# Kernel tuning notes

Measured on AMD Instinct MI355X. Metric: run time of the kernel, lower is better.

Reference implementation:

```python
import jax, jax.numpy as jnp
import numpy as np

B, N2, N3, N4 = 128, 1024, 256, 64
D, H, MLP = 128, 2, 512
EPS = 1e-5


def _sinusoid(n, d):
    pos = np.arange(n, dtype=np.float64)[:, None]
    i = np.arange(d)[None, :]
    ang = pos / np.power(10000.0, 2.0 * (i // 2) / d)
    tab = np.where(i % 2 == 0, np.sin(ang), np.cos(ang))
    return jnp.asarray(tab[None], jnp.float32)  # [1, n, d]


def setup_inputs() -> dict:
    key = jax.random.key(0)
    ks = jax.random.split(key, 16)
    s = 0.02
    inp = {
        "f2": jax.random.normal(ks[0], (B, N2, D), jnp.float32),
        "f3": jax.random.normal(ks[1], (B, N3, D), jnp.float32),
        "f4": jax.random.normal(ks[2], (B, N4, D), jnp.float32),
        "pe2": _sinusoid(N2, D),
        "pe3": _sinusoid(N3, D),
        "pe4": _sinusoid(N4, D),
        "ln1_w": jnp.ones((D,), jnp.float32), "ln1_b": jnp.zeros((D,), jnp.float32),
        "ln2_w": jnp.ones((D,), jnp.float32), "ln2_b": jnp.zeros((D,), jnp.float32),
        "ln3_w": jnp.ones((D,), jnp.float32), "ln3_b": jnp.zeros((D,), jnp.float32),
        "ln4_w": jnp.ones((D,), jnp.float32), "ln4_b": jnp.zeros((D,), jnp.float32),
        "q1_w": s * jax.random.normal(ks[3], (D, D), jnp.float32), "q1_b": jnp.zeros((D,), jnp.float32),
        "k1_w": s * jax.random.normal(ks[4], (D, D), jnp.float32), "k1_b": jnp.zeros((D,), jnp.float32),
        "v1_w": s * jax.random.normal(ks[5], (D, D), jnp.float32), "v1_b": jnp.zeros((D,), jnp.float32),
        "q2_w": s * jax.random.normal(ks[6], (D, D), jnp.float32), "q2_b": jnp.zeros((D,), jnp.float32),
        "k2_w": s * jax.random.normal(ks[7], (D, D), jnp.float32), "k2_b": jnp.zeros((D,), jnp.float32),
        "v2_w": s * jax.random.normal(ks[8], (D, D), jnp.float32), "v2_b": jnp.zeros((D,), jnp.float32),
        "rp_w": s * jax.random.normal(ks[9], (2 * D, D), jnp.float32), "rp_b": jnp.zeros((D,), jnp.float32),
        "ff1_w": s * jax.random.normal(ks[10], (D, MLP), jnp.float32), "ff1_b": jnp.zeros((MLP,), jnp.float32),
        "ff2_w": s * jax.random.normal(ks[11], (MLP, D), jnp.float32), "ff2_b": jnp.zeros((D,), jnp.float32),
    }
    return inp


def _ln(x, w, b):
    m = x.mean(-1, keepdims=True)
    v = ((x - m) ** 2).mean(-1, keepdims=True)  # biased var, matches torch LayerNorm
    return (x - m) * jax.lax.rsqrt(v + EPS) * w + b


def _eff_attn(q, k, v):
    # q: [B,Nq,D]; k,v: [B,Nk,D]. Linear (efficient) attention:
    # softmax over tokens for Q, softmax over head channels for K.
    b, nq, _ = q.shape
    nk = k.shape[1]
    dh = D // H
    qs = jax.nn.softmax(q.reshape(b, nq, H, dh), axis=1)   # dim=2 in [B,C,N] layout == token axis
    ks = jax.nn.softmax(k.reshape(b, nk, H, dh), axis=3)   # dim=1 in [B,C,N] layout == channel axis
    vs = v.reshape(b, nk, H, dh)
    ctx = jnp.einsum('bnhd,bnhe->bhde', ks, vs)            # [B,H,dh,dh] context
    out = jnp.einsum('bhde,bnhd->bnhe', ctx, qs)           # [B,Nq,H,dh]
    return out.reshape(b, nq, D)


def reference(f2, f3, f4, pe2, pe3, pe4,
              ln1_w, ln1_b, ln2_w, ln2_b, ln3_w, ln3_b, ln4_w, ln4_b,
              q1_w, q1_b, k1_w, k1_b, v1_w, v1_b,
              q2_w, q2_b, k2_w, k2_b, v2_w, v2_b,
              rp_w, rp_b, ff1_w, ff1_b, ff2_w, ff2_b):
    f2n = _ln(f2, ln1_w, ln1_b)
    f3n = _ln(f3, ln2_w, ln2_b)
    f4n = _ln(f4, ln3_w, ln3_b)
    q1 = (f2n + pe2) @ q1_w + q1_b
    q2 = (f2n + pe2) @ q2_w + q2_b
    k3 = (f3n + pe3) @ k1_w + k1_b
    v3 = f3n @ v1_w + v1_b
    k4 = (f4n + pe4) @ k2_w + k2_b
    v4 = f4n @ v2_w + v2_b
    a32 = _eff_attn(q1, k3, v3)
    a42 = _eff_attn(q2, k4, v4)
    attn = jnp.concatenate([a32, a42], axis=-1) @ rp_w + rp_b
    x = f2 + attn
    h = _ln(x, ln4_w, ln4_b)
    h = jax.nn.gelu(h @ ff1_w + ff1_b, approximate=False) @ ff2_w + ff2_b
    return x + h
```

## Files before the change

kernel.cpp:

```cpp
#include <hip/hip_runtime.h>
#include <hip/hip_bf16.h>
#include <math.h>

#define BB 128
#define NN2 1024
#define NN3 256
#define NN4 64
#define DD 128
#define MLPD 512
#define EPSF 1e-5f

typedef short bf16x8 __attribute__((ext_vector_type(8)));
typedef float f32x4 __attribute__((ext_vector_type(4)));

__device__ inline ushort f2b(float x) {
    __hip_bfloat16 h = __float2bfloat16(x);
    return __builtin_bit_cast(ushort, h);
}
__device__ inline float b2f(ushort u) {
    unsigned int v = ((unsigned int)u) << 16;
    return __builtin_bit_cast(float, v);
}
__device__ inline float gelu_f(float u) {
    float t = 0.7978845608f * u + 0.0356774081f * (u * u * u);
    float e = __expf(2.f * t);
    return u - u * __builtin_amdgcn_rcpf(e + 1.f);
}

#define MFMA(a, b, c) __builtin_amdgcn_mfma_f32_16x16x32_bf16((a), (b), (c), 0, 0, 0)

__device__ inline char* swad(char* base, int row, int bytecol, int strideB) {
    return base + (size_t)row * strideB + ((bytecol) ^ ((row & 7) << 4));
}

template <int STRIDE>
__device__ inline void ln_stage(const float* __restrict__ x, long base,
                                const float* __restrict__ w, const float* __restrict__ b,
                                ushort xn[][STRIDE], int t)
{
    int r = t >> 3, l8 = t & 7;
    const float4* xr4 = reinterpret_cast<const float4*>(x + (base + r) * DD);
    float4 v[4];
#pragma unroll
    for (int j = 0; j < 4; ++j) v[j] = xr4[l8 * 4 + j];
    float s = 0.f;
#pragma unroll
    for (int j = 0; j < 4; ++j) s += v[j].x + v[j].y + v[j].z + v[j].w;
#pragma unroll
    for (int m = 1; m <= 4; m <<= 1) s += __shfl_xor(s, m, 64);
    float mean = s * (1.f / 128.f);
    float s2 = 0.f;
#pragma unroll
    for (int j = 0; j < 4; ++j) {
        v[j].x -= mean; v[j].y -= mean; v[j].z -= mean; v[j].w -= mean;
        s2 += v[j].x * v[j].x + v[j].y * v[j].y + v[j].z * v[j].z + v[j].w * v[j].w;
    }
#pragma unroll
    for (int m = 1; m <= 4; m <<= 1) s2 += __shfl_xor(s2, m, 64);
    float rstd = rsqrtf(s2 * (1.f / 128.f) + EPSF);
    int c0 = l8 * 16;
#pragma unroll
    for (int j = 0; j < 4; ++j) {
        int c = c0 + j * 4;
        float o0 = v[j].x * rstd * w[c] + b[c];
        float o1 = v[j].y * rstd * w[c + 1] + b[c + 1];
        float o2 = v[j].z * rstd * w[c + 2] + b[c + 2];
        float o3 = v[j].w * rstd * w[c + 3] + b[c + 3];
        uint2 uu;
        uu.x = (unsigned int)f2b(o0) | ((unsigned int)f2b(o1) << 16);
        uu.y = (unsigned int)f2b(o2) | ((unsigned int)f2b(o3) << 16);
        *reinterpret_cast<uint2*>(&xn[r][c]) = uu;
    }
}

__global__ __launch_bounds__(256) void prep_tw(
    const float* __restrict__ q1w, const float* __restrict__ q2w,
    const float* __restrict__ k1w, const float* __restrict__ v1w,
    const float* __restrict__ k2w, const float* __restrict__ v2w,
    const float* __restrict__ ff1w, const float* __restrict__ ff2w,
    const float* __restrict__ rpw,
    ushort* __restrict__ Wqt, ushort* __restrict__ Wkv3t, ushort* __restrict__ Wkv4t,
    ushort* __restrict__ W1t, ushort* __restrict__ W2t, ushort* __restrict__ RpT)
{
    __shared__ ushort trans[4][64][88];
    int w = threadIdx.x >> 6, l = threadIdx.x & 63;
    int tile = blockIdx.x * 4 + w;
    const float* src; ushort* dst; int K, N, tk, tn;
    if (tile < 24) {
        int job = tile >> 2, rel = tile & 3;
        K = 128; N = 128; tk = rel >> 1; tn = rel & 1;
        if      (job == 0) { src = q1w; dst = Wqt; }
        else if (job == 1) { src = q2w; dst = Wqt + 16384; }
        else if (job == 2) { src = k1w; dst = Wkv3t; }
        else if (job == 3) { src = v1w; dst = Wkv3t + 16384; }
        else if (job == 4) { src = k2w; dst = Wkv4t; }
        else               { src = v2w; dst = Wkv4t + 16384; }
    } else if (tile < 40) {
        int rel = tile - 24; src = ff1w; dst = W1t; K = 128; N = 512; tk = rel >> 3; tn = rel & 7;
    } else if (tile < 56) {
        int rel = tile - 40; src = ff2w; dst = W2t; K = 512; N = 128; tk = rel >> 1; tn = rel & 1;
    } else {
        int rel = tile - 56; src = rpw; dst = RpT; K = 256; N = 128; tk = rel >> 1; tn = rel & 1;
    }
    int k0 = tk * 64, n0 = tn * 64;
#pragma unroll
    for (int i = 0; i < 16; ++i) {
        int kr = i * 4 + (l >> 4), nc = (l & 15) * 4;
        float4 v = *reinterpret_cast<const float4*>(&src[(size_t)(k0 + kr) * N + n0 + nc]);
        trans[w][nc + 0][kr] = f2b(v.x);
        trans[w][nc + 1][kr] = f2b(v.y);
        trans[w][nc + 2][kr] = f2b(v.z);
        trans[w][nc + 3][kr] = f2b(v.w);
    }
    __syncthreads();
#pragma unroll
    for (int i = 0; i < 8; ++i) {
        int nr = i * 8 + (l >> 3), c0 = (l & 7) * 8;
        int4 vv = *reinterpret_cast<const int4*>(&trans[w][nr][c0]);
        *reinterpret_cast<int4*>(&dst[(size_t)(n0 + nr) * K + k0 + c0]) = vv;
    }
}

__global__ __launch_bounds__(256) void prep_pe2(
    const float* __restrict__ pe2, const float* __restrict__ pe3, const float* __restrict__ pe4,
    const ushort* __restrict__ Wqt, const ushort* __restrict__ Wkv3t, const ushort* __restrict__ Wkv4t,
    const float* __restrict__ q1b, const float* __restrict__ q2b,
    const float* __restrict__ k1b, const float* __restrict__ v1b,
    const float* __restrict__ k2b, const float* __restrict__ v2b,
    float* __restrict__ peq, float* __restrict__ pekv3, float* __restrict__ pekv4)
{
    __shared__ ushort xn[32][136];
    int bid = blockIdx.x, t = threadIdx.x;
    const float* pe; const ushort* Wt; float* outp; const float* bl; const float* bh; int hiDot; long tb;
    if (bid < 32)      { pe = pe2; Wt = Wqt;   outp = peq;   bl = q1b; bh = q2b; hiDot = 1; tb = (long)bid * 32; }
    else if (bid < 40) { pe = pe3; Wt = Wkv3t; outp = pekv3; bl = k1b; bh = v1b; hiDot = 0; tb = (long)(bid - 32) * 32; }
    else               { pe = pe4; Wt = Wkv4t; outp = pekv4; bl = k2b; bh = v2b; hiDot = 0; tb = (long)(bid - 40) * 32; }
    {
        int r = t >> 3, l8 = t & 7;
        const float4* pr = reinterpret_cast<const float4*>(pe + (tb + r) * 128);
#pragma unroll
        for (int j = 0; j < 4; ++j) {
            float4 v = pr[l8 * 4 + j];
            int c = l8 * 16 + j * 4;
            uint2 uu;
            uu.x = (unsigned int)f2b(v.x) | ((unsigned int)f2b(v.y) << 16);
            uu.y = (unsigned int)f2b(v.z) | ((unsigned int)f2b(v.w) << 16);
            *reinterpret_cast<uint2*>(&xn[r][c]) = uu;
        }
    }
    __syncthreads();
    int w = t >> 6, l = t & 63, l15 = l & 15, rg = l >> 4;
    f32x4 acc[2][4];
#pragma unroll
    for (int m = 0; m < 2; ++m)
#pragma unroll
        for (int n = 0; n < 4; ++n) acc[m][n] = (f32x4){0.f, 0.f, 0.f, 0.f};
#pragma unroll
    for (int kc = 0; kc < 4; ++kc) {
        bf16x8 a0 = *reinterpret_cast<const bf16x8*>(&xn[l15][kc * 32 + rg * 8]);
        bf16x8 a1 = *reinterpret_cast<const bf16x8*>(&xn[16 + l15][kc * 32 + rg * 8]);
#pragma unroll
        for (int nt = 0; nt < 4; ++nt) {
            bf16x8 bfr = *reinterpret_cast<const bf16x8*>(
                &Wt[(size_t)(w * 64 + nt * 16 + l15) * 128 + kc * 32 + rg * 8]);
            acc[0][nt] = MFMA(a0, bfr, acc[0][nt]);
            acc[1][nt] = MFMA(a1, bfr, acc[1][nt]);
        }
    }
#pragma unroll
    for (int mt = 0; mt < 2; ++mt)
#pragma unroll
        for (int j = 0; j < 4; ++j) {
            int row = mt * 16 + rg * 4 + j;
#pragma unroll
            for (int nt = 0; nt < 4; ++nt) {
                int col = w * 64 + nt * 16 + l15;
                float bias = (col < 128) ? bl[col] : bh[col - 128];
                float v = bias + ((col < 128 || hiDot) ? acc[mt][nt][j] : 0.f);
                outp[(tb + row) * 256 + col] = v;
            }
        }
}

__global__ __launch_bounds__(256) void kv_mfma(
    const float* __restrict__ x, const float* __restrict__ lnw, const float* __restrict__ lnb,
    const ushort* __restrict__ Wt, const float* __restrict__ pekv,
    ushort* __restrict__ kst, ushort* __restrict__ vst, int ntok, int ntok_shift)
{
    __shared__ ushort xn[32][136];
    __shared__ ushort trans[4][64][40];
    int t = threadIdx.x;
    long base = (long)blockIdx.x * 32;
    ln_stage<136>(x, base, lnw, lnb, xn, t);
    __syncthreads();
    int w = t >> 6, l = t & 63, l15 = l & 15, rg = l >> 4;
    f32x4 acc[2][4];
#pragma unroll
    for (int m = 0; m < 2; ++m)
#pragma unroll
        for (int n = 0; n < 4; ++n) acc[m][n] = (f32x4){0.f, 0.f, 0.f, 0.f};
#pragma unroll
    for (int kc = 0; kc < 4; ++kc) {
        bf16x8 a0 = *reinterpret_cast<const bf16x8*>(&xn[l15][kc * 32 + rg * 8]);
        bf16x8 a1 = *reinterpret_cast<const bf16x8*>(&xn[16 + l15][kc * 32 + rg * 8]);
#pragma unroll
        for (int nt = 0; nt < 4; ++nt) {
            bf16x8 bfr = *reinterpret_cast<const bf16x8*>(
                &Wt[(size_t)(w * 64 + nt * 16 + l15) * 128 + kc * 32 + rg * 8]);
            acc[0][nt] = MFMA(a0, bfr, acc[0][nt]);
            acc[1][nt] = MFMA(a1, bfr, acc[1][nt]);
        }
    }
    float val[2][4][4];
#pragma unroll
    for (int mt = 0; mt < 2; ++mt)
#pragma unroll
        for (int j = 0; j < 4; ++j) {
            int row = mt * 16 + rg * 4 + j;
            int tok = (int)((base + row) & (ntok - 1));
#pragma unroll
            for (int nt = 0; nt < 4; ++nt) {
                int col = w * 64 + nt * 16 + l15;
                val[mt][nt][j] = acc[mt][nt][j] + pekv[tok * 256 + col];
            }
        }
    if (w < 2) {
#pragma unroll
        for (int mt = 0; mt < 2; ++mt)
#pragma unroll
            for (int j = 0; j < 4; ++j) {
                float mx = val[mt][0][j];
#pragma unroll
                for (int nt = 1; nt < 4; ++nt) mx = fmaxf(mx, val[mt][nt][j]);
#pragma unroll
                for (int m = 1; m <= 8; m <<= 1) mx = fmaxf(mx, __shfl_xor(mx, m, 64));
                float e[4], se = 0.f;
#pragma unroll
                for (int nt = 0; nt < 4; ++nt) { e[nt] = __expf(val[mt][nt][j] - mx); se += e[nt]; }
#pragma unroll
                for (int m = 1; m <= 8; m <<= 1) se += __shfl_xor(se, m, 64);
                float inv = 1.f / se;
#pragma unroll
                for (int nt = 0; nt < 4; ++nt) val[mt][nt][j] = e[nt] * inv;
            }
    }
#pragma unroll
    for (int mt = 0; mt < 2; ++mt)
#pragma unroll
        for (int nt = 0; nt < 4; ++nt)
#pragma unroll
            for (int j = 0; j < 4; ++j)
                trans[w][nt * 16 + l15][mt * 16 + rg * 4 + j] = f2b(val[mt][nt][j]);
    __syncthreads();
    ushort* dst = (w < 2) ? kst : vst;
    int h = w & 1;
    int b = (int)(base >> ntok_shift);
    int tok0 = (int)(base & (ntok - 1));
    long o = (((long)(b * 2 + h) * 64 + l) * ntok + tok0);
    const int4* src = reinterpret_cast<const int4*>(&trans[w][l][0]);
    int4* dp = reinterpret_cast<int4*>(&dst[o]);
#pragma unroll
    for (int i = 0; i < 4; ++i) dp[i] = src[i];
}

__global__ __launch_bounds__(64) void ctx_mfma(
    const ushort* __restrict__ kst3, const ushort* __restrict__ vst3,
    const ushort* __restrict__ kst4, const ushort* __restrict__ vst4,
    ushort* __restrict__ ctxn)
{
    int bid = blockIdx.x;
    int b = bid >> 2, g = bid & 3;
    const ushort* ks; const ushort* vs; int ntok;
    if (g < 2) { ntok = 256; ks = kst3 + (long)(b * 2 + g) * 64 * 256; vs = vst3 + (long)(b * 2 + g) * 64 * 256; }
    else       { ntok = 64;  ks = kst4 + (long)(b * 2 + (g - 2)) * 64 * 64; vs = vst4 + (long)(b * 2 + (g - 2)) * 64 * 64; }
    int l = threadIdx.x, l15 = l & 15, rg = l >> 4;
    f32x4 acc[4][4];
#pragma unroll
    for (int m = 0; m < 4; ++m)
#pragma unroll
        for (int n = 0; n < 4; ++n) acc[m][n] = (f32x4){0.f, 0.f, 0.f, 0.f};
    for (int kc = 0; kc < (ntok >> 5); ++kc) {
        bf16x8 a[4];
#pragma unroll
        for (int mt = 0; mt < 4; ++mt)
            a[mt] = *reinterpret_cast<const bf16x8*>(&ks[(size_t)(mt * 16 + l15) * ntok + kc * 32 + rg * 8]);
#pragma unroll
        for (int nt = 0; nt < 4; ++nt) {
            bf16x8 bfr = *reinterpret_cast<const bf16x8*>(&vs[(size_t)(nt * 16 + l15) * ntok + kc * 32 + rg * 8]);
#pragma unroll
            for (int mt = 0; mt < 4; ++mt) acc[mt][nt] = MFMA(a[mt], bfr, acc[mt][nt]);
        }
    }
#pragma unroll
    for (int mt = 0; mt < 4; ++mt)
#pragma unroll
        for (int nt = 0; nt < 4; ++nt)
#pragma unroll
            for (int j = 0; j < 4; ++j)
                ctxn[((long)bid * 64 + mt * 16 + rg * 4 + j) * 64 + nt * 16 + l15] = f2b(acc[mt][nt][j]);
}

__global__ __launch_bounds__(512) void q_mfma(
    const float* __restrict__ f2, const float* __restrict__ lnw, const float* __restrict__ lnb,
    const ushort* __restrict__ Wqt, const float* __restrict__ peq,
    ushort* __restrict__ qexp, float* __restrict__ partial)
{
    __shared__ ushort xn[64][136];
    __shared__ ushort qt[64][264];
    int t = threadIdx.x;
    long base = (long)blockIdx.x * 64;
    ln_stage<136>(f2, base, lnw, lnb, xn, t);
    __syncthreads();
    int w = t >> 6, l = t & 63, l15 = l & 15, rg = l >> 4;
    f32x4 acc[4][2];
#pragma unroll
    for (int m = 0; m < 4; ++m)
#pragma unroll
        for (int n = 0; n < 2; ++n) acc[m][n] = (f32x4){0.f, 0.f, 0.f, 0.f};
#pragma unroll
    for (int kc = 0; kc < 4; ++kc) {
        bf16x8 a[4];
#pragma unroll
        for (int m = 0; m < 4; ++m)
            a[m] = *reinterpret_cast<const bf16x8*>(&xn[m * 16 + l15][kc * 32 + rg * 8]);
#pragma unroll
        for (int nt = 0; nt < 2; ++nt) {
            bf16x8 bfr = *reinterpret_cast<const bf16x8*>(
                &Wqt[(size_t)(w * 32 + nt * 16 + l15) * 128 + kc * 32 + rg * 8]);
#pragma unroll
            for (int m = 0; m < 4; ++m) acc[m][nt] = MFMA(a[m], bfr, acc[m][nt]);
        }
    }
    float esum[2] = {0.f, 0.f};
#pragma unroll
    for (int m = 0; m < 4; ++m)
#pragma unroll
        for (int j = 0; j < 4; ++j) {
            int row = m * 16 + rg * 4 + j;
            int tok = (int)((base + row) & (NN2 - 1));
#pragma unroll
            for (int nt = 0; nt < 2; ++nt) {
                int col = w * 32 + nt * 16 + l15;
                float v = acc[m][nt][j] + peq[tok * 256 + col];
                float e = __expf(v);
                qt[row][col] = f2b(e);
                esum[nt] += e;
            }
        }
#pragma unroll
    for (int nt = 0; nt < 2; ++nt) {
        esum[nt] += __shfl_xor(esum[nt], 16, 64);
        esum[nt] += __shfl_xor(esum[nt], 32, 64);
    }
    if (rg == 0) {
        int bidx = blockIdx.x >> 4, chunk = blockIdx.x & 15;
#pragma unroll
        for (int nt = 0; nt < 2; ++nt)
            partial[(size_t)(bidx * 16 + chunk) * 256 + w * 32 + nt * 16 + l15] = esum[nt];
    }
    __syncthreads();
    {
        int r = t >> 3, c0 = (t & 7) * 32;
        const int4* sp = reinterpret_cast<const int4*>(&qt[r][c0]);
        int4* dst = reinterpret_cast<int4*>(&qexp[(base + r) * 256 + c0]);
#pragma unroll
        for (int i = 0; i < 4; ++i) dst[i] = sp[i];
    }
}

__global__ __launch_bounds__(256) void scale_rp(
    const float* __restrict__ partial, const ushort* __restrict__ ctxn,
    const ushort* __restrict__ RpT, ushort* __restrict__ MbT)
{
    __shared__ float rsv[256];
    int b = blockIdx.x, t = threadIdx.x;
    {
        float s = 0.f;
        for (int ch = 0; ch < 16; ++ch) s += partial[((size_t)b * 16 + ch) * 256 + t];
        rsv[t] = 1.f / s;
    }
    __syncthreads();
    int w = t >> 6, l = t & 63, l15 = l & 15, rg = l >> 4;
    const ushort* cb = ctxn + ((long)(b * 4 + w)) * 4096;
    bf16x8 a[4][2];
#pragma unroll
    for (int m = 0; m < 4; ++m) {
        float sc = rsv[w * 64 + m * 16 + l15];
#pragma unroll
        for (int kc = 0; kc < 2; ++kc) {
            bf16x8 raw = *reinterpret_cast<const bf16x8*>(
                &cb[(size_t)(m * 16 + l15) * 64 + kc * 32 + rg * 8]);
#pragma unroll
            for (int i = 0; i < 8; ++i)
                raw[i] = (short)f2b(b2f((ushort)raw[i]) * sc);
            a[m][kc] = raw;
        }
    }
#pragma unroll
    for (int nt = 0; nt < 8; ++nt) {
        f32x4 acc[4];
#pragma unroll
        for (int m = 0; m < 4; ++m) acc[m] = (f32x4){0.f, 0.f, 0.f, 0.f};
#pragma unroll
        for (int kc = 0; kc < 2; ++kc) {
            bf16x8 bfr = *reinterpret_cast<const bf16x8*>(
                &RpT[(size_t)(nt * 16 + l15) * 256 + w * 64 + kc * 32 + rg * 8]);
#pragma unroll
            for (int m = 0; m < 4; ++m) acc[m] = MFMA(a[m][kc], bfr, acc[m]);
        }
        int n = nt * 16 + l15;
#pragma unroll
        for (int m = 0; m < 4; ++m) {
            unsigned int u0 = (unsigned int)f2b(acc[m][0]) | ((unsigned int)f2b(acc[m][1]) << 16);
            unsigned int u1 = (unsigned int)f2b(acc[m][2]) | ((unsigned int)f2b(acc[m][3]) << 16);
            uint2 uu; uu.x = u0; uu.y = u1;
            *reinterpret_cast<uint2*>(&MbT[((long)b * 128 + n) * 256 + w * 64 + m * 16 + rg * 4]) = uu;
        }
    }
}

__global__ __launch_bounds__(512, 4) void attn_mlp(
    const ushort* __restrict__ qexp, const ushort* __restrict__ MbT,
    const float* __restrict__ rpb, const float* __restrict__ f2,
    const float* __restrict__ lnw, const float* __restrict__ lnb,
    const ushort* __restrict__ W1t, const float* __restrict__ ff1b,
    const ushort* __restrict__ W2t, const float* __restrict__ ff2b,
    float* __restrict__ out)
{
    __shared__ __align__(16) char smem[32768];
    char* XN = smem;
    char* R2 = smem + 16384;
    float* Ps = reinterpret_cast<float*>(R2);
    float* Pq = reinterpret_cast<float*>(R2 + 2048);
    float* MR = reinterpret_cast<float*>(R2 + 4096);
    float* RR = reinterpret_cast<float*>(R2 + 4352);
    int t = threadIdx.x;
    long base = (long)blockIdx.x * 64;
    int b = blockIdx.x >> 4;
    int w = t >> 6, l = t & 63, l15 = l & 15, rg = l >> 4;
    int col = w * 16 + l15;

    f32x4 accC[4];
#pragma unroll
    for (int m = 0; m < 4; ++m) accC[m] = (f32x4){0.f, 0.f, 0.f, 0.f};
    {
        const ushort* mb = MbT + (long)b * 128 * 256;
#pragma unroll
        for (int h = 0; h < 2; ++h) {
            {
                int sr = t >> 3, sc = (t & 7) * 32;
                const char* src = (const char*)qexp + (base + sr) * 512 + h * 256 + sc;
                int4 v0 = *reinterpret_cast<const int4*>(src);
                int4 v1 = *reinterpret_cast<const int4*>(src + 16);
                *reinterpret_cast<int4*>(swad(R2, sr, sc, 256)) = v0;
                *reinterpret_cast<int4*>(swad(R2, sr, sc + 16, 256)) = v1;
            }
            __syncthreads();
#pragma unroll
            for (int kc = 0; kc < 4; ++kc) {
                bf16x8 bfr = *reinterpret_cast<const bf16x8*>(
                    &mb[(size_t)col * 256 + h * 128 + kc * 32 + rg * 8]);
#pragma unroll
                for (int m = 0; m < 4; ++m) {
                    bf16x8 a = *reinterpret_cast<const bf16x8*>(
                        swad(R2, m * 16 + l15, (kc * 32 + rg * 8) * 2, 256));
                    accC[m] = MFMA(a, bfr, accC[m]);
                }
            }
            __syncthreads();
        }
    }

    float xres[4][4];
    {
        float bias = rpb[col];
#pragma unroll
        for (int m = 0; m < 4; ++m)
#pragma unroll
            for (int j = 0; j < 4; ++j) {
                int row = m * 16 + rg * 4 + j;
                long g = (base + row) * 128 + col;
                float xv = f2[g] + accC[m][j] + bias;
                xres[m][j] = xv;
                float s = xv, q = xv * xv;
#pragma unroll
                for (int msk = 1; msk <= 8; msk <<= 1) {
                    s += __shfl_xor(s, msk, 64);
                    q += __shfl_xor(q, msk, 64);
                }
                if (l15 == 0) { Ps[row * 8 + w] = s; Pq[row * 8 + w] = q; }
            }
    }
    __syncthreads();
    if (t < 64) {
        float4 s0 = *reinterpret_cast<float4*>(&Ps[t * 8]);
        float4 s1 = *reinterpret_cast<float4*>(&Ps[t * 8 + 4]);
        float4 q0 = *reinterpret_cast<float4*>(&Pq[t * 8]);
        float4 q1 = *reinterpret_cast<float4*>(&Pq[t * 8 + 4]);
        float s = s0.x + s0.y + s0.z + s0.w + s1.x + s1.y + s1.z + s1.w;
        float q = q0.x + q0.y + q0.z + q0.w + q1.x + q1.y + q1.z + q1.w;
        float mean = s * (1.f / 128.f);
        float var = q * (1.f / 128.f) - mean * mean;
        MR[t] = mean;
        RR[t] = rsqrtf(var + EPSF);
    }
    __syncthreads();
    {
        float lw = lnw[col], lb = lnb[col];
#pragma unroll
        for (int m = 0; m < 4; ++m)
#pragma unroll
            for (int j = 0; j < 4; ++j) {
                int row = m * 16 + rg * 4 + j;
                float o = (xres[m][j] - MR[row]) * RR[row] * lw + lb;
                *reinterpret_cast<ushort*>(swad(XN, row, col * 2, 256)) = f2b(o);
            }
    }
    __syncthreads();

    f32x4 accF[4];
#pragma unroll
    for (int m = 0; m < 4; ++m) accF[m] = (f32x4){0.f, 0.f, 0.f, 0.f};
#pragma unroll
    for (int q = 0; q < 4; ++q) {
        {
            f32x4 acc[4];
#pragma unroll
            for (int m = 0; m < 4; ++m) acc[m] = (f32x4){0.f, 0.f, 0.f, 0.f};
#pragma unroll
            for (int kc = 0; kc < 4; ++kc) {
                bf16x8 bfr = *reinterpret_cast<const bf16x8*>(
                    &W1t[(size_t)(q * 128 + col) * 128 + kc * 32 + rg * 8]);
#pragma unroll
                for (int m = 0; m < 4; ++m) {
                    bf16x8 a = *reinterpret_cast<const bf16x8*>(
                        swad(XN, m * 16 + l15, (kc * 32 + rg * 8) * 2, 256));
                    acc[m] = MFMA(a, bfr, acc[m]);
                }
            }
            float b1 = ff1b[q * 128 + col];
#pragma unroll
            for (int m = 0; m < 4; ++m)
#pragma unroll
                for (int j = 0; j < 4; ++j)
                    *reinterpret_cast<ushort*>(swad(R2, m * 16 + rg * 4 + j, col * 2, 256))
                        = f2b(gelu_f(acc[m][j] + b1));
        }
        __syncthreads();
#pragma unroll
        for (int kc = 0; kc < 4; ++kc) {
            bf16x8 bfr = *reinterpret_cast<const bf16x8*>(
                &W2t[(size_t)col * 512 + q * 128 + kc * 32 + rg * 8]);
#pragma unroll
            for (int m = 0; m < 4; ++m) {
                bf16x8 a = *reinterpret_cast<const bf16x8*>(
                    swad(R2, m * 16 + l15, (kc * 32 + rg * 8) * 2, 256));
                accF[m] = MFMA(a, bfr, accF[m]);
            }
        }
        if (q < 3) __syncthreads();
    }
    {
        float b2 = ff2b[col];
#pragma unroll
        for (int m = 0; m < 4; ++m)
#pragma unroll
            for (int j = 0; j < 4; ++j) {
                int row = m * 16 + rg * 4 + j;
                long g = (base + row) * 128 + col;
                out[g] = xres[m][j] + accF[m][j] + b2;
            }
    }
}

extern "C" void kernel_launch(void* const* d_in, const int* in_sizes, int n_in,
                              void* d_out, int out_size, void* d_ws, size_t ws_size,
                              hipStream_t stream) {
    const float* f2   = (const float*)d_in[0];
    const float* f3   = (const float*)d_in[1];
    const float* f4   = (const float*)d_in[2];
    const float* pe2  = (const float*)d_in[3];
    const float* pe3  = (const float*)d_in[4];
    const float* pe4  = (const float*)d_in[5];
    const float* ln1w = (const float*)d_in[6];
    const float* ln1b = (const float*)d_in[7];
    const float* ln2w = (const float*)d_in[8];
    const float* ln2b = (const float*)d_in[9];
    const float* ln3w = (const float*)d_in[10];
    const float* ln3b = (const float*)d_in[11];
    const float* ln4w = (const float*)d_in[12];
    const float* ln4b = (const float*)d_in[13];
    const float* q1w  = (const float*)d_in[14];
    const float* q1b  = (const float*)d_in[15];
    const float* k1w  = (const float*)d_in[16];
    const float* k1b  = (const float*)d_in[17];
    const float* v1w  = (const float*)d_in[18];
    const float* v1b  = (const float*)d_in[19];
    const float* q2w  = (const float*)d_in[20];
    const float* q2b  = (const float*)d_in[21];
    const float* k2w  = (const float*)d_in[22];
    const float* k2b  = (const float*)d_in[23];
    const float* v2w  = (const float*)d_in[24];
    const float* v2b  = (const float*)d_in[25];
    const float* rpw  = (const float*)d_in[26];
    const float* rpb  = (const float*)d_in[27];
    const float* ff1w = (const float*)d_in[28];
    const float* ff1b = (const float*)d_in[29];
    const float* ff2w = (const float*)d_in[30];
    const float* ff2b = (const float*)d_in[31];

    char* ws = (char*)d_ws;
    size_t off = 0;
    ushort* qexp  = (ushort*)(ws + off); off += (size_t)BB * NN2 * 256 * 2;
    ushort* kst3  = (ushort*)(ws + off); off += (size_t)BB * 2 * 64 * NN3 * 2;
    ushort* vst3  = (ushort*)(ws + off); off += (size_t)BB * 2 * 64 * NN3 * 2;
    ushort* kst4  = (ushort*)(ws + off); off += (size_t)BB * 2 * 64 * NN4 * 2;
    ushort* vst4  = (ushort*)(ws + off); off += (size_t)BB * 2 * 64 * NN4 * 2;
    ushort* ctxn  = (ushort*)(ws + off); off += (size_t)BB * 4 * 64 * 64 * 2;
    ushort* MbT   = (ushort*)(ws + off); off += (size_t)BB * 128 * 256 * 2;
    ushort* Wqt   = (ushort*)(ws + off); off += 256 * 128 * 2;
    ushort* Wkv3t = (ushort*)(ws + off); off += 256 * 128 * 2;
    ushort* Wkv4t = (ushort*)(ws + off); off += 256 * 128 * 2;
    ushort* W1t   = (ushort*)(ws + off); off += 512 * 128 * 2;
    ushort* W2t   = (ushort*)(ws + off); off += 128 * 512 * 2;
    ushort* RpT   = (ushort*)(ws + off); off += 128 * 256 * 2;
    float*  peq   = (float*)(ws + off);  off += (size_t)NN2 * 256 * 4;
    float*  pekv3 = (float*)(ws + off);  off += (size_t)NN3 * 256 * 4;
    float*  pekv4 = (float*)(ws + off);  off += (size_t)NN4 * 256 * 4;
    float*  partial = (float*)(ws + off); off += (size_t)BB * 16 * 256 * 4;

    prep_tw<<<16, 256, 0, stream>>>(q1w, q2w, k1w, v1w, k2w, v2w, ff1w, ff2w, rpw,
                                    Wqt, Wkv3t, Wkv4t, W1t, W2t, RpT);
    prep_pe2<<<42, 256, 0, stream>>>(pe2, pe3, pe4, Wqt, Wkv3t, Wkv4t,
                                     q1b, q2b, k1b, v1b, k2b, v2b, peq, pekv3, pekv4);
    kv_mfma<<<BB * NN3 / 32, 256, 0, stream>>>(f3, ln2w, ln2b, Wkv3t, pekv3, kst3, vst3, NN3, 8);
    kv_mfma<<<BB * NN4 / 32, 256, 0, stream>>>(f4, ln3w, ln3b, Wkv4t, pekv4, kst4, vst4, NN4, 6);
    ctx_mfma<<<BB * 4, 64, 0, stream>>>(kst3, vst3, kst4, vst4, ctxn);
    q_mfma<<<BB * NN2 / 64, 512, 0, stream>>>(f2, ln1w, ln1b, Wqt, peq, qexp, partial);
    scale_rp<<<BB, 256, 0, stream>>>(partial, ctxn, RpT, MbT);
    attn_mlp<<<BB * NN2 / 64, 512, 0, stream>>>(qexp, MbT, rpb, f2,
                                                ln4w, ln4b, W1t, ff1b, W2t, ff2b, (float*)d_out);
}
```

Baseline: 247.3 us.

## Merge prep kernels, fuse K/V projection launches, swizzle q_mfma shared memory

Weight transposition and positional-embedding projection now run in one prep launch. The PE projection is a plain per-thread fp32 dot product, which removes the dependency on the transposed weights, and the two K/V projection launches are merged into one. The q_mfma shared buffers are repacked into a 32KB XOR-swizzled layout with no padding, and launch bounds are set to allow 4 blocks per CU. The swizzle generalises to wider row strides. The intent is fewer launches, fewer LDS bank conflicts and higher occupancy, at the cost of a slower scalar PE projection and an extra barrier.

```diff
diff --git a/kernel.cpp b/kernel.cpp
--- a/kernel.cpp
+++ b/kernel.cpp
@@ -30,7 +30,7 @@
 #define MFMA(a, b, c) __builtin_amdgcn_mfma_f32_16x16x32_bf16((a), (b), (c), 0, 0, 0)
 
 __device__ inline char* swad(char* base, int row, int bytecol, int strideB) {
-    return base + (size_t)row * strideB + ((bytecol) ^ ((row & 7) << 4));
+    return base + (size_t)row * strideB + ((bytecol) ^ ((row << 4) & (strideB - 16)));
 }
 
 template <int STRIDE>
@@ -73,124 +73,151 @@
     }
 }
 
-__global__ __launch_bounds__(256) void prep_tw(
+__device__ inline void ln_stage_s(const float* __restrict__ x, long base,
+                                  const float* __restrict__ w, const float* __restrict__ b,
+                                  char* R, int t)
+{
+    int r = t >> 3, l8 = t & 7;
+    const float4* xr4 = reinterpret_cast<const float4*>(x + (base + r) * DD);
+    float4 v[4];
+#pragma unroll
+    for (int j = 0; j < 4; ++j) v[j] = xr4[l8 * 4 + j];
+    float s = 0.f;
+#pragma unroll
+    for (int j = 0; j < 4; ++j) s += v[j].x + v[j].y + v[j].z + v[j].w;
+#pragma unroll
+    for (int m = 1; m <= 4; m <<= 1) s += __shfl_xor(s, m, 64);
+    float mean = s * (1.f / 128.f);
+    float s2 = 0.f;
+#pragma unroll
+    for (int j = 0; j < 4; ++j) {
+        v[j].x -= mean; v[j].y -= mean; v[j].z -= mean; v[j].w -= mean;
+        s2 += v[j].x * v[j].x + v[j].y * v[j].y + v[j].z * v[j].z + v[j].w * v[j].w;
+    }
+#pragma unroll
+    for (int m = 1; m <= 4; m <<= 1) s2 += __shfl_xor(s2, m, 64);
+    float rstd = rsqrtf(s2 * (1.f / 128.f) + EPSF);
+    int c0 = l8 * 16;
+#pragma unroll
+    for (int j = 0; j < 4; ++j) {
+        int c = c0 + j * 4;
+        float o0 = v[j].x * rstd * w[c] + b[c];
+        float o1 = v[j].y * rstd * w[c + 1] + b[c + 1];
+        float o2 = v[j].z * rstd * w[c + 2] + b[c + 2];
+        float o3 = v[j].w * rstd * w[c + 3] + b[c + 3];
+        uint2 uu;
+        uu.x = (unsigned int)f2b(o0) | ((unsigned int)f2b(o1) << 16);
+        uu.y = (unsigned int)f2b(o2) | ((unsigned int)f2b(o3) << 16);
+        *reinterpret_cast<uint2*>(swad(R, r, c * 2, 256)) = uu;
+    }
+}
+
+__global__ __launch_bounds__(256) void prep_all(
     const float* __restrict__ q1w, const float* __restrict__ q2w,
     const float* __restrict__ k1w, const float* __restrict__ v1w,
     const float* __restrict__ k2w, const float* __restrict__ v2w,
     const float* __restrict__ ff1w, const float* __restrict__ ff2w,
     const float* __restrict__ rpw,
-    ushort* __restrict__ Wqt, ushort* __restrict__ Wkv3t, ushort* __restrict__ Wkv4t,
-    ushort* __restrict__ W1t, ushort* __restrict__ W2t, ushort* __restrict__ RpT)
-{
-    __shared__ ushort trans[4][64][88];
-    int w = threadIdx.x >> 6, l = threadIdx.x & 63;
-    int tile = blockIdx.x * 4 + w;
-    const float* src; ushort* dst; int K, N, tk, tn;
-    if (tile < 24) {
-        int job = tile >> 2, rel = tile & 3;
-        K = 128; N = 128; tk = rel >> 1; tn = rel & 1;
-        if      (job == 0) { src = q1w; dst = Wqt; }
-        else if (job == 1) { src = q2w; dst = Wqt + 16384; }
-        else if (job == 2) { src = k1w; dst = Wkv3t; }
-        else if (job == 3) { src = v1w; dst = Wkv3t + 16384; }
-        else if (job == 4) { src = k2w; dst = Wkv4t; }
-        else               { src = v2w; dst = Wkv4t + 16384; }
-    } else if (tile < 40) {
-        int rel = tile - 24; src = ff1w; dst = W1t; K = 128; N = 512; tk = rel >> 3; tn = rel & 7;
-    } else if (tile < 56) {
-        int rel = tile - 40; src = ff2w; dst = W2t; K = 512; N = 128; tk = rel >> 1; tn = rel & 1;
-    } else {
-        int rel = tile - 56; src = rpw; dst = RpT; K = 256; N = 128; tk = rel >> 1; tn = rel & 1;
-    }
-    int k0 = tk * 64, n0 = tn * 64;
-#pragma unroll
-    for (int i = 0; i < 16; ++i) {
-        int kr = i * 4 + (l >> 4), nc = (l & 15) * 4;
-        float4 v = *reinterpret_cast<const float4*>(&src[(size_t)(k0 + kr) * N + n0 + nc]);
-        trans[w][nc + 0][kr] = f2b(v.x);
-        trans[w][nc + 1][kr] = f2b(v.y);
-        trans[w][nc + 2][kr] = f2b(v.z);
-        trans[w][nc + 3][kr] = f2b(v.w);
-    }
-    __syncthreads();
-#pragma unroll
-    for (int i = 0; i < 8; ++i) {
-        int nr = i * 8 + (l >> 3), c0 = (l & 7) * 8;
-        int4 vv = *reinterpret_cast<const int4*>(&trans[w][nr][c0]);
-        *reinterpret_cast<int4*>(&dst[(size_t)(n0 + nr) * K + k0 + c0]) = vv;
-    }
-}
-
-__global__ __launch_bounds__(256) void prep_pe2(
     const float* __restrict__ pe2, const float* __restrict__ pe3, const float* __restrict__ pe4,
-    const ushort* __restrict__ Wqt, const ushort* __restrict__ Wkv3t, const ushort* __restrict__ Wkv4t,
     const float* __restrict__ q1b, const float* __restrict__ q2b,
     const float* __restrict__ k1b, const float* __restrict__ v1b,
     const float* __restrict__ k2b, const float* __restrict__ v2b,
+    ushort* __restrict__ Wqt, ushort* __restrict__ Wkv3t, ushort* __restrict__ Wkv4t,
+    ushort* __restrict__ W1t, ushort* __restrict__ W2t, ushort* __restrict__ RpT,
     float* __restrict__ peq, float* __restrict__ pekv3, float* __restrict__ pekv4)
 {
-    __shared__ ushort xn[32][136];
-    int bid = blockIdx.x, t = threadIdx.x;
-    const float* pe; const ushort* Wt; float* outp; const float* bl; const float* bh; int hiDot; long tb;
-    if (bid < 32)      { pe = pe2; Wt = Wqt;   outp = peq;   bl = q1b; bh = q2b; hiDot = 1; tb = (long)bid * 32; }
-    else if (bid < 40) { pe = pe3; Wt = Wkv3t; outp = pekv3; bl = k1b; bh = v1b; hiDot = 0; tb = (long)(bid - 32) * 32; }
-    else               { pe = pe4; Wt = Wkv4t; outp = pekv4; bl = k2b; bh = v2b; hiDot = 0; tb = (long)(bid - 40) * 32; }
-    {
-        int r = t >> 3, l8 = t & 7;
-        const float4* pr = reinterpret_cast<const float4*>(pe + (tb + r) * 128);
-#pragma unroll
-        for (int j = 0; j < 4; ++j) {
-            float4 v = pr[l8 * 4 + j];
-            int c = l8 * 16 + j * 4;
-            uint2 uu;
-            uu.x = (unsigned int)f2b(v.x) | ((unsigned int)f2b(v.y) << 16);
-            uu.y = (unsigned int)f2b(v.z) | ((unsigned int)f2b(v.w) << 16);
-            *reinterpret_cast<uint2*>(&xn[r][c]) = uu;
-        }
-    }
-    __syncthreads();
-    int w = t >> 6, l = t & 63, l15 = l & 15, rg = l >> 4;
-    f32x4 acc[2][4];
-#pragma unroll
-    for (int m = 0; m < 2; ++m)
-#pragma unroll
-        for (int n = 0; n < 4; ++n) acc[m][n] = (f32x4){0.f, 0.f, 0.f, 0.f};
-#pragma unroll
-    for (int kc = 0; kc < 4; ++kc) {
-        bf16x8 a0 = *reinterpret_cast<const bf16x8*>(&xn[l15][kc * 32 + rg * 8]);
-        bf16x8 a1 = *reinterpret_cast<const bf16x8*>(&xn[16 + l15][kc * 32 + rg * 8]);
-#pragma unroll
-        for (int nt = 0; nt < 4; ++nt) {
-            bf16x8 bfr = *reinterpret_cast<const bf16x8*>(
-                &Wt[(size_t)(w * 64 + nt * 16 + l15) * 128 + kc * 32 + rg * 8]);
-            acc[0][nt] = MFMA(a0, bfr, acc[0][nt]);
-            acc[1][nt] = MFMA(a1, bfr, acc[1][nt]);
-        }
-    }
-#pragma unroll
-    for (int mt = 0; mt < 2; ++mt)
-#pragma unroll
-        for (int j = 0; j < 4; ++j) {
-            int row = mt * 16 + rg * 4 + j;
-#pragma unroll
-            for (int nt = 0; nt < 4; ++nt) {
-                int col = w * 64 + nt * 16 + l15;
-                float bias = (col < 128) ? bl[col] : bh[col - 128];
-                float v = bias + ((col < 128 || hiDot) ? acc[mt][nt][j] : 0.f);
-                outp[(tb + row) * 256 + col] = v;
-            }
-        }
-}
-
-__global__ __launch_bounds__(256) void kv_mfma(
-    const float* __restrict__ x, const float* __restrict__ lnw, const float* __restrict__ lnb,
-    const ushort* __restrict__ Wt, const float* __restrict__ pekv,
-    ushort* __restrict__ kst, ushort* __restrict__ vst, int ntok, int ntok_shift)
+    __shared__ ushort trans[4][64][88];
+    if (blockIdx.x < 16) {
+        int w = threadIdx.x >> 6, l = threadIdx.x & 63;
+        int tile = blockIdx.x * 4 + w;
+        const float* src; ushort* dst; int K, N, tk, tn;
+        if (tile < 24) {
+            int job = tile >> 2, rel = tile & 3;
+            K = 128; N = 128; tk = rel >> 1; tn = rel & 1;
+            if      (job == 0) { src = q1w; dst = Wqt; }
+            else if (job == 1) { src = q2w; dst = Wqt + 16384; }
+            else if (job == 2) { src = k1w; dst = Wkv3t; }
+            else if (job == 3) { src = v1w; dst = Wkv3t + 16384; }
+            else if (job == 4) { src = k2w; dst = Wkv4t; }
+            else               { src = v2w; dst = Wkv4t + 16384; }
+        } else if (tile < 40) {
+            int rel = tile - 24; src = ff1w; dst = W1t; K = 128; N = 512; tk = rel >> 3; tn = rel & 7;
+        } else if (tile < 56) {
+            int rel = tile - 40; src = ff2w; dst = W2t; K = 512; N = 128; tk = rel >> 1; tn = rel & 1;
+        } else {
+            int rel = tile - 56; src = rpw; dst = RpT; K = 256; N = 128; tk = rel >> 1; tn = rel & 1;
+        }
+        int k0 = tk * 64, n0 = tn * 64;
+#pragma unroll
+        for (int i = 0; i < 16; ++i) {
+            int kr = i * 4 + (l >> 4), nc = (l & 15) * 4;
+            float4 v = *reinterpret_cast<const float4*>(&src[(size_t)(k0 + kr) * N + n0 + nc]);
+            trans[w][nc + 0][kr] = f2b(v.x);
+            trans[w][nc + 1][kr] = f2b(v.y);
+            trans[w][nc + 2][kr] = f2b(v.z);
+            trans[w][nc + 3][kr] = f2b(v.w);
+        }
+        __syncthreads();
+#pragma unroll
+        for (int i = 0; i < 8; ++i) {
+            int nr = i * 8 + (l >> 3), c0 = (l & 7) * 8;
+            int4 vv = *reinterpret_cast<const int4*>(&trans[w][nr][c0]);
+            *reinterpret_cast<int4*>(&dst[(size_t)(n0 + nr) * K + k0 + c0]) = vv;
+        }
+        return;
+    }
+    int bid = blockIdx.x - 16;
+    int c = threadIdx.x, cc = c & 127;
+    if (bid < 1024) {
+        const float* pr = pe2 + bid * 128;
+        const float* w = (c < 128) ? q1w : q2w;
+        float acc = (c < 128) ? q1b[cc] : q2b[cc];
+        for (int k = 0; k < 128; ++k) acc += pr[k] * w[k * 128 + cc];
+        peq[bid * 256 + c] = acc;
+    } else if (bid < 1280) {
+        int tok = bid - 1024;
+        const float* pr = pe3 + tok * 128;
+        float acc;
+        if (c < 128) {
+            acc = k1b[cc];
+            for (int k = 0; k < 128; ++k) acc += pr[k] * k1w[k * 128 + cc];
+        } else acc = v1b[cc];
+        pekv3[tok * 256 + c] = acc;
+    } else {
+        int tok = bid - 1280;
+        const float* pr = pe4 + tok * 128;
+        float acc;
+        if (c < 128) {
+            acc = k2b[cc];
+            for (int k = 0; k < 128; ++k) acc += pr[k] * k2w[k * 128 + cc];
+        } else acc = v2b[cc];
+        pekv4[tok * 256 + c] = acc;
+    }
+}
+
+__global__ __launch_bounds__(256) void kv_both(
+    const float* __restrict__ f3, const float* __restrict__ f4,
+    const float* __restrict__ ln2w, const float* __restrict__ ln2b,
+    const float* __restrict__ ln3w, const float* __restrict__ ln3b,
+    const ushort* __restrict__ Wkv3t, const ushort* __restrict__ Wkv4t,
+    const float* __restrict__ pekv3, const float* __restrict__ pekv4,
+    ushort* __restrict__ kst3, ushort* __restrict__ vst3,
+    ushort* __restrict__ kst4, ushort* __restrict__ vst4)
 {
     __shared__ ushort xn[32][136];
     __shared__ ushort trans[4][64][40];
+    const float* x; const float* lnw; const float* lnb; const ushort* Wt; const float* pekv;
+    ushort* kst; ushort* vst; int ntok, ntok_shift; long base;
+    if (blockIdx.x < 1024) {
+        x = f3; lnw = ln2w; lnb = ln2b; Wt = Wkv3t; pekv = pekv3;
+        kst = kst3; vst = vst3; ntok = NN3; ntok_shift = 8;
+        base = (long)blockIdx.x * 32;
+    } else {
+        x = f4; lnw = ln3w; lnb = ln3b; Wt = Wkv4t; pekv = pekv4;
+        kst = kst4; vst = vst4; ntok = NN4; ntok_shift = 6;
+        base = (long)(blockIdx.x - 1024) * 32;
+    }
     int t = threadIdx.x;
-    long base = (long)blockIdx.x * 32;
     ln_stage<136>(x, base, lnw, lnb, xn, t);
     __syncthreads();
     int w = t >> 6, l = t & 63, l15 = l & 15, rg = l >> 4;
@@ -300,16 +327,17 @@
                 ctxn[((long)bid * 64 + mt * 16 + rg * 4 + j) * 64 + nt * 16 + l15] = f2b(acc[mt][nt][j]);
 }
 
-__global__ __launch_bounds__(512) void q_mfma(
+__global__ __launch_bounds__(512, 4) void q_mfma(
     const float* __restrict__ f2, const float* __restrict__ lnw, const float* __restrict__ lnb,
     const ushort* __restrict__ Wqt, const float* __restrict__ peq,
     ushort* __restrict__ qexp, float* __restrict__ partial)
 {
-    __shared__ ushort xn[64][136];
-    __shared__ ushort qt[64][264];
+    __shared__ __align__(16) char smem[32768];
+    char* XN = smem + 16384;
+    char* QT = smem;
     int t = threadIdx.x;
     long base = (long)blockIdx.x * 64;
-    ln_stage<136>(f2, base, lnw, lnb, xn, t);
+    ln_stage_s(f2, base, lnw, lnb, XN, t);
     __syncthreads();
     int w = t >> 6, l = t & 63, l15 = l & 15, rg = l >> 4;
     f32x4 acc[4][2];
@@ -322,7 +350,7 @@
         bf16x8 a[4];
 #pragma unroll
         for (int m = 0; m < 4; ++m)
-            a[m] = *reinterpret_cast<const bf16x8*>(&xn[m * 16 + l15][kc * 32 + rg * 8]);
+            a[m] = *reinterpret_cast<const bf16x8*>(swad(XN, m * 16 + l15, (kc * 32 + rg * 8) * 2, 256));
 #pragma unroll
         for (int nt = 0; nt < 2; ++nt) {
             bf16x8 bfr = *reinterpret_cast<const bf16x8*>(
@@ -331,6 +359,7 @@
             for (int m = 0; m < 4; ++m) acc[m][nt] = MFMA(a[m], bfr, acc[m][nt]);
         }
     }
+    __syncthreads();
     float esum[2] = {0.f, 0.f};
 #pragma unroll
     for (int m = 0; m < 4; ++m)
@@ -341,9 +370,8 @@
 #pragma unroll
             for (int nt = 0; nt < 2; ++nt) {
                 int col = w * 32 + nt * 16 + l15;
-                float v = acc[m][nt][j] + peq[tok * 256 + col];
-                float e = __expf(v);
-                qt[row][col] = f2b(e);
+                float e = __expf(acc[m][nt][j] + peq[tok * 256 + col]);
+                *reinterpret_cast<ushort*>(swad(QT, row, col * 2, 512)) = f2b(e);
                 esum[nt] += e;
             }
         }
@@ -360,11 +388,13 @@
     }
     __syncthreads();
     {
-        int r = t >> 3, c0 = (t & 7) * 32;
-        const int4* sp = reinterpret_cast<const int4*>(&qt[r][c0]);
-        int4* dst = reinterpret_cast<int4*>(&qexp[(base + r) * 256 + c0]);
-#pragma unroll
-        for (int i = 0; i < 4; ++i) dst[i] = sp[i];
+        int r = t >> 3, c0 = (t & 7) * 64;
+        char* dst = (char*)qexp + (base + r) * 512 + c0;
+#pragma unroll
+        for (int i = 0; i < 4; ++i) {
+            int4 vv = *reinterpret_cast<const int4*>(swad(QT, r, c0 + i * 16, 512));
+            *reinterpret_cast<int4*>(dst + i * 16) = vv;
+        }
     }
 }
 
@@ -629,12 +659,12 @@
     float*  pekv4 = (float*)(ws + off);  off += (size_t)NN4 * 256 * 4;
     float*  partial = (float*)(ws + off); off += (size_t)BB * 16 * 256 * 4;
 
-    prep_tw<<<16, 256, 0, stream>>>(q1w, q2w, k1w, v1w, k2w, v2w, ff1w, ff2w, rpw,
-                                    Wqt, Wkv3t, Wkv4t, W1t, W2t, RpT);
-    prep_pe2<<<42, 256, 0, stream>>>(pe2, pe3, pe4, Wqt, Wkv3t, Wkv4t,
-                                     q1b, q2b, k1b, v1b, k2b, v2b, peq, pekv3, pekv4);
-    kv_mfma<<<BB * NN3 / 32, 256, 0, stream>>>(f3, ln2w, ln2b, Wkv3t, pekv3, kst3, vst3, NN3, 8);
-    kv_mfma<<<BB * NN4 / 32, 256, 0, stream>>>(f4, ln3w, ln3b, Wkv4t, pekv4, kst4, vst4, NN4, 6);
+    prep_all<<<16 + 1344, 256, 0, stream>>>(q1w, q2w, k1w, v1w, k2w, v2w, ff1w, ff2w, rpw,
+                                            pe2, pe3, pe4, q1b, q2b, k1b, v1b, k2b, v2b,
+                                            Wqt, Wkv3t, Wkv4t, W1t, W2t, RpT,
+                                            peq, pekv3, pekv4);
+    kv_both<<<1280, 256, 0, stream>>>(f3, f4, ln2w, ln2b, ln3w, ln3b, Wkv3t, Wkv4t,
+                                      pekv3, pekv4, kst3, vst3, kst4, vst4);
     ctx_mfma<<<BB * 4, 64, 0, stream>>>(kst3, vst3, kst4, vst4, ctxn);
     q_mfma<<<BB * NN2 / 64, 512, 0, stream>>>(f2, ln1w, ln1b, Wqt, peq, qexp, partial);
     scale_rp<<<BB, 256, 0, stream>>>(partial, ctxn, RpT, MbT);
```

After: 236.9 us. 4.2% less time.
